# Optimization experiments

Hardware: AMD Instinct MI355X
Metric: run time of the kernel (lower is better)

The kernel has to match this reference:

```python
import jax, jax.numpy as jnp
import numpy as np

B, N, DS, DP, H, DH = 2, 512, 384, 128, 16, 64
MAX_SEQ = 2048
DI = H * DH  # inner attention dim = 1024
LN_EPS = 1e-5


def setup_inputs() -> dict:
    key = jax.random.key(0)
    ks = jax.random.split(key, 10)
    s = 0.02  # param init scale
    return {
        "single_repr": jax.random.normal(ks[0], (B, N, DS), jnp.float32),
        "pairwise_repr": jax.random.normal(ks[1], (B, N, N, DP), jnp.float32),
        "ln_gamma": jnp.ones((DP,), jnp.float32),
        "ln_beta": jnp.zeros((DP,), jnp.float32),
        "w_bias": jax.random.normal(ks[2], (DP, H), jnp.float32) * s,
        "attn_bias_bias": jax.random.normal(ks[3], (MAX_SEQ, MAX_SEQ), jnp.float32) * s,
        "w_q": jax.random.normal(ks[4], (DS, DI), jnp.float32) * s,
        "w_k": jax.random.normal(ks[5], (DS, DI), jnp.float32) * s,
        "w_v": jax.random.normal(ks[6], (DS, DI), jnp.float32) * s,
        "w_g": jax.random.normal(ks[7], (DS, DI), jnp.float32) * s,
        "w_o": jax.random.normal(ks[8], (DI, DS), jnp.float32) * s,
    }


def reference(single_repr, pairwise_repr, ln_gamma, ln_beta, w_bias,
              attn_bias_bias, w_q, w_k, w_v, w_g, w_o):
    b, n, _ = single_repr.shape
    # LayerNorm over pairwise feature dim, then project to per-head bias
    mu = pairwise_repr.mean(-1, keepdims=True)
    var = pairwise_repr.var(-1, keepdims=True)
    pr = (pairwise_repr - mu) * jax.lax.rsqrt(var + LN_EPS) * ln_gamma + ln_beta
    # ... i j h -> ... h i j, plus learned positional bias slice
    attn_bias = jnp.einsum('bijd,dh->bhij', pr, w_bias) + attn_bias_bias[:n, :n]

    # multi-head attention with additive per-head bias and sigmoid gating
    q = (single_repr @ w_q).reshape(b, n, H, DH).transpose(0, 2, 1, 3)  # bhnd
    k = (single_repr @ w_k).reshape(b, n, H, DH).transpose(0, 2, 1, 3)
    v = (single_repr @ w_v).reshape(b, n, H, DH).transpose(0, 2, 1, 3)
    scale = DH ** -0.5
    scores = jnp.einsum('bhid,bhjd->bhij', q, k) * scale + attn_bias
    attn = jax.nn.softmax(scores, axis=-1)
    o = jnp.einsum('bhij,bhjd->bhid', attn, v)
    o = o.transpose(0, 2, 1, 3).reshape(b, n, DI)
    gates = jax.nn.sigmoid(single_repr @ w_g)
    return (o * gates) @ w_o
```

## Files before the change

kernel.cpp:

```cpp
#include <hip/hip_runtime.h>
#include <hip/hip_bf16.h>

#define B_ 2
#define N_ 512
#define DS_ 384
#define DP_ 128
#define H_ 16
#define DH_ 64
#define DI_ 1024
#define MAXSEQ 2048
#define PAD 8

typedef float f32x4 __attribute__((ext_vector_type(4)));
typedef short bf16x8 __attribute__((ext_vector_type(8)));
typedef unsigned int u32x4 __attribute__((ext_vector_type(4)));

__device__ __forceinline__ unsigned short f2b(float f) {
    unsigned int u = __builtin_bit_cast(unsigned int, f);
    u += 0x7FFFu + ((u >> 16) & 1u);
    return (unsigned short)(u >> 16);
}
__device__ __forceinline__ float b2f(unsigned short s) {
    unsigned int u = ((unsigned int)s) << 16;
    return __builtin_bit_cast(float, u);
}

#define SW(row, bc) ((bc) ^ (((row) & 7) << 4))

__global__ __launch_bounds__(256) void k_pre(const float* __restrict__ pw,
                                             const float* __restrict__ abb,
                                             const float* __restrict__ gamma,
                                             const float* __restrict__ beta,
                                             const float* __restrict__ wb,
                                             const float* __restrict__ wq,
                                             const float* __restrict__ wk,
                                             const float* __restrict__ wv,
                                             const float* __restrict__ wg,
                                             const float* __restrict__ wo,
                                             unsigned short* __restrict__ Wt,
                                             unsigned short* __restrict__ Wot,
                                             unsigned short* __restrict__ biasP) {
    __shared__ float Xs[64 * 128];
    __shared__ float rsum[4][16] __attribute__((aligned(16)));
    __shared__ float rsq[4][16] __attribute__((aligned(16)));
    int bid = blockIdx.x;
    int t = threadIdx.x;

    if (bid >= 8192) {
        int tid = bid - 8192;
        int z = tid / 384, r = tid % 384;
        const float* in; unsigned short* out; int C, Rr, c0, r0;
        if (z < 4) {
            in = (z == 0) ? wq : (z == 1) ? wk : (z == 2) ? wv : wg;
            out = Wt + (long)z * 1024 * 384;
            C = 1024; Rr = 384;
            c0 = (r & 31) * 32; r0 = (r >> 5) * 32;
        } else {
            in = wo; out = Wot; C = 384; Rr = 1024;
            c0 = (r % 12) * 32; r0 = (r / 12) * 32;
        }
        float (*tile)[33] = (float(*)[33])Xs;
        int tx = t & 31, ty = t >> 5;
        #pragma unroll
        for (int i = ty; i < 32; i += 8)
            tile[i][tx] = in[(long)(r0 + i) * C + (c0 + tx)];
        __syncthreads();
        #pragma unroll
        for (int i = ty; i < 32; i += 8)
            out[(long)(c0 + i) * Rr + (r0 + tx)] = f2b(tile[tx][i]);
        return;
    }

    int w = t >> 6, lane = t & 63;
    int lane15 = lane & 15, kg = lane >> 4;
    long p0 = (long)bid * 64;
    int i_blk = (int)((p0 >> 9) & (N_ - 1));
    int j0 = (int)(p0 & (N_ - 1));
    long bb = p0 >> 18;

    const char* src = (const char*)(pw + (p0 << 7));
    char* lds = (char*)Xs;
    #pragma unroll
    for (int c = 0; c < 8; ++c) {
        int L = c * 4096 + t * 16;
        int row = L >> 9, b = L & 511;
        u32x4 v = __builtin_nontemporal_load((const u32x4*)(src + L));
        *(u32x4*)(lds + (row << 9) + (b ^ ((row & 7) << 4))) = v;
    }

    float shp = 0.f, thp = 0.f;
    bf16x8 gb[4];
    #pragma unroll
    for (int kk = 0; kk < 4; ++kk) {
        bf16x8 a;
        unsigned short* ap = (unsigned short*)&a;
        #pragma unroll
        for (int e = 0; e < 8; ++e) {
            int d = kk * 32 + kg * 8 + e;
            float wv_ = wb[d * 16 + lane15];
            float gv = gamma[d];
            ap[e] = f2b(gv * wv_);
            shp = fmaf(gv, wv_, shp);
            thp = fmaf(beta[d], wv_, thp);
        }
        gb[kk] = a;
    }
    shp += __shfl_xor(shp, 16); shp += __shfl_xor(shp, 32);
    thp += __shfl_xor(thp, 16); thp += __shfl_xor(thp, 32);
    float sh = shp, th = thp;
    __syncthreads();

    int row = w * 16 + lane15;
    const char* rbase = lds + (row << 9);
    int sw = (lane15 & 7) << 4;
    f32x4 xa[4], xb4[4];
    #pragma unroll
    for (int kk = 0; kk < 4; ++kk) {
        int b0 = kk * 128 + kg * 32;
        xa[kk]  = *(const f32x4*)(rbase + ((b0) ^ sw));
        xb4[kk] = *(const f32x4*)(rbase + ((b0 + 16) ^ sw));
    }
    float s = 0.f, q = 0.f;
    #pragma unroll
    for (int kk = 0; kk < 4; ++kk) {
        s += xa[kk][0] + xa[kk][1] + xa[kk][2] + xa[kk][3];
        s += xb4[kk][0] + xb4[kk][1] + xb4[kk][2] + xb4[kk][3];
        #pragma unroll
        for (int e = 0; e < 4; ++e) {
            q = fmaf(xa[kk][e], xa[kk][e], q);
            q = fmaf(xb4[kk][e], xb4[kk][e], q);
        }
    }
    s += __shfl_xor(s, 16); s += __shfl_xor(s, 32);
    q += __shfl_xor(q, 16); q += __shfl_xor(q, 32);
    if (lane < 16) { rsum[w][lane15] = s; rsq[w][lane15] = q; }

    f32x4 acc = {};
    #pragma unroll
    for (int kk = 0; kk < 4; ++kk) {
        bf16x8 a;
        unsigned short* ap = (unsigned short*)&a;
        ap[0] = f2b(xa[kk][0]);  ap[1] = f2b(xa[kk][1]);
        ap[2] = f2b(xa[kk][2]);  ap[3] = f2b(xa[kk][3]);
        ap[4] = f2b(xb4[kk][0]); ap[5] = f2b(xb4[kk][1]);
        ap[6] = f2b(xb4[kk][2]); ap[7] = f2b(xb4[kk][3]);
        acc = __builtin_amdgcn_mfma_f32_16x16x32_bf16(a, gb[kk], acc, 0, 0, 0);
    }
    int jr = w * 16 + kg * 4;
    float4 rs = *(const float4*)&rsum[w][kg * 4];
    float4 rq = *(const float4*)&rsq[w][kg * 4];
    float4 av = *(const float4*)(abb + (long)i_blk * MAXSEQ + j0 + jr);
    unsigned short* planeBase = biasP + ((bb * H_ + lane15) * N_ + i_blk) * N_ + j0;
    ushort4 res;
    float mu, var;
    mu = rs.x * (1.f / DP_); var = fmaf(rq.x, 1.f / DP_, -mu * mu);
    res.x = f2b(fmaf(rsqrtf(var + 1e-5f), acc[0] - mu * sh, th + av.x));
    mu = rs.y * (1.f / DP_); var = fmaf(rq.y, 1.f / DP_, -mu * mu);
    res.y = f2b(fmaf(rsqrtf(var + 1e-5f), acc[1] - mu * sh, th + av.y));
    mu = rs.z * (1.f / DP_); var = fmaf(rq.z, 1.f / DP_, -mu * mu);
    res.z = f2b(fmaf(rsqrtf(var + 1e-5f), acc[2] - mu * sh, th + av.z));
    mu = rs.w * (1.f / DP_); var = fmaf(rq.w, 1.f / DP_, -mu * mu);
    res.w = f2b(fmaf(rsqrtf(var + 1e-5f), acc[3] - mu * sh, th + av.w));
    *(ushort4*)(planeBase + jr) = res;
}

__global__ __launch_bounds__(256) void k_proj(const float* __restrict__ X,
                                              const unsigned short* __restrict__ Wt,
                                              unsigned short* __restrict__ Qb,
                                              unsigned short* __restrict__ Kb,
                                              unsigned short* __restrict__ Vt,
                                              unsigned short* __restrict__ Xg) {
    __shared__ unsigned short As[64][64 + PAD];
    __shared__ unsigned short Bs[128][64 + PAD];
    int m0 = blockIdx.x * 64;
    int n0 = blockIdx.y * 128;
    int t = threadIdx.x;
    int wave = t >> 6, lane = t & 63;
    int wr = wave >> 1, wc = wave & 1;
    int lane15 = lane & 15, kg = lane >> 4;
    int rA = t >> 2, qA = t & 3;
    int rB = t >> 1, hB = t & 1;
    f32x4 acc[2][4] = {};
    for (int k0 = 0; k0 < DS_; k0 += 64) {
        __syncthreads();
        {
            const float4* srcA = (const float4*)(X + (long)(m0 + rA) * DS_ + k0 + qA * 16);
            unsigned short* dstA = &As[rA][qA * 16];
            #pragma unroll
            for (int ii = 0; ii < 4; ++ii) {
                float4 v = srcA[ii];
                dstA[ii * 4 + 0] = f2b(v.x); dstA[ii * 4 + 1] = f2b(v.y);
                dstA[ii * 4 + 2] = f2b(v.z); dstA[ii * 4 + 3] = f2b(v.w);
            }
            const uint4* srcB = (const uint4*)(Wt + (long)(n0 + rB) * DS_ + k0 + hB * 32);
            uint4* dstB = (uint4*)&Bs[rB][hB * 32];
            dstB[0] = srcB[0]; dstB[1] = srcB[1]; dstB[2] = srcB[2]; dstB[3] = srcB[3];
        }
        __syncthreads();
        #pragma unroll
        for (int ks = 0; ks < 2; ++ks) {
            bf16x8 a[2], bbv[4];
            #pragma unroll
            for (int mf = 0; mf < 2; ++mf)
                a[mf] = *(const bf16x8*)&As[wr * 32 + mf * 16 + lane15][ks * 32 + kg * 8];
            #pragma unroll
            for (int nf = 0; nf < 4; ++nf)
                bbv[nf] = *(const bf16x8*)&Bs[wc * 64 + nf * 16 + lane15][ks * 32 + kg * 8];
            #pragma unroll
            for (int mf = 0; mf < 2; ++mf)
                #pragma unroll
                for (int nf = 0; nf < 4; ++nf)
                    acc[mf][nf] = __builtin_amdgcn_mfma_f32_16x16x32_bf16(a[mf], bbv[nf], acc[mf][nf], 0, 0, 0);
        }
    }
    int p = n0 >> 10;
    int lgrp = lane >> 4;
    #pragma unroll
    for (int mf = 0; mf < 2; ++mf) {
        #pragma unroll
        for (int nf = 0; nf < 4; ++nf) {
            int col = n0 + wc * 64 + nf * 16 + lane15;
            int ch = col & 1023;
            int h = ch >> 6, dh = ch & 63;
            int row0 = m0 + wr * 32 + mf * 16 + lgrp * 4;
            if (p == 0 || p == 1) {
                unsigned short* base = (p == 0) ? Qb : Kb;
                float scl = (p == 0) ? 0.125f : 1.0f;
                #pragma unroll
                for (int rr = 0; rr < 4; ++rr) {
                    int rowx = row0 + rr;
                    int b = rowx >> 9, n = rowx & 511;
                    base[(((long)(b * 16 + h)) * 512 + n) * 64 + dh] = f2b(acc[mf][nf][rr] * scl);
                }
            } else if (p == 2) {
                int b = row0 >> 9, n = row0 & 511;
                ushort4 v;
                v.x = f2b(acc[mf][nf][0]); v.y = f2b(acc[mf][nf][1]);
                v.z = f2b(acc[mf][nf][2]); v.w = f2b(acc[mf][nf][3]);
                *(ushort4*)&Vt[(((long)(b * 16 + h)) * 64 + dh) * 512 + n] = v;
            } else {
                #pragma unroll
                for (int rr = 0; rr < 4; ++rr) {
                    int rowx = row0 + rr;
                    Xg[(long)rowx * 1024 + ch] = f2b(acc[mf][nf][rr]);
                }
            }
        }
    }
}

__global__ __launch_bounds__(512) void k_flash(const unsigned short* __restrict__ Qb,
                                               const unsigned short* __restrict__ Kb,
                                               const unsigned short* __restrict__ Vt,
                                               const unsigned short* __restrict__ biasP,
                                               const unsigned short* __restrict__ Xg,
                                               unsigned short* __restrict__ Og) {
    __shared__ unsigned short Kt[2][64][64];
    __shared__ unsigned short Vs[2][64][64];
    __shared__ unsigned short Bt[2][64][64];
    __shared__ char PsOscr[16384];
    __shared__ float Mscr[4][16], Lscr[4][16];
    unsigned short (*Ps)[16][64] = (unsigned short(*)[16][64])PsOscr;
    float (*Oscr)[16][64] = (float(*)[16][64])PsOscr;
    int bh = blockIdx.y;
    int b = bh >> 4, h = bh & 15;
    int i0 = blockIdx.x * 64;
    int t = threadIdx.x, w = t >> 6, lane = t & 63;
    int g = w & 3, jg = w >> 2;
    int lane15 = lane & 15, lgrp = lane >> 4;
    int tl = t & 255;
    int rs_ = tl >> 3, cs_ = tl & 7;

    bf16x8 qf[2];
    #pragma unroll
    for (int kk = 0; kk < 2; ++kk)
        qf[kk] = *(const bf16x8*)&Qb[((long)bh * 512 + i0 + g * 16 + lane15) * 64 + kk * 32 + lgrp * 8];

    float m_run = -1e30f, l_run = 0.f;
    f32x4 o[4] = {};

    for (int jtl = 0; jtl < 4; ++jtl) {
        int j0 = (jg * 4 + jtl) * 64;
        __syncthreads();
        {
            int r2 = rs_ + 32;
            *(uint4*)((char*)&Kt[jg][rs_][0] + SW(rs_, cs_ * 16)) =
                *(const uint4*)&Kb[((long)bh * 512 + j0 + rs_) * 64 + cs_ * 8];
            *(uint4*)((char*)&Vs[jg][rs_][0] + SW(rs_, cs_ * 16)) =
                *(const uint4*)&Vt[((long)bh * 64 + rs_) * 512 + j0 + cs_ * 8];
            *(uint4*)((char*)&Bt[jg][rs_][0] + SW(rs_, cs_ * 16)) =
                *(const uint4*)&biasP[((long)bh * 512 + i0 + rs_) * 512 + j0 + cs_ * 8];
            *(uint4*)((char*)&Kt[jg][r2][0] + SW(r2, cs_ * 16)) =
                *(const uint4*)&Kb[((long)bh * 512 + j0 + r2) * 64 + cs_ * 8];
            *(uint4*)((char*)&Vs[jg][r2][0] + SW(r2, cs_ * 16)) =
                *(const uint4*)&Vt[((long)bh * 64 + r2) * 512 + j0 + cs_ * 8];
            *(uint4*)((char*)&Bt[jg][r2][0] + SW(r2, cs_ * 16)) =
                *(const uint4*)&biasP[((long)bh * 512 + i0 + r2) * 512 + j0 + cs_ * 8];
        }
        __syncthreads();

        f32x4 s[4];
        #pragma unroll
        for (int nf = 0; nf < 4; ++nf) {
            f32x4 z = {};
            #pragma unroll
            for (int kk = 0; kk < 2; ++kk) {
                bf16x8 af = *(const bf16x8*)((const char*)&Kt[jg][nf * 16 + lane15][0] +
                                             SW(lane15, kk * 64 + lgrp * 16));
                z = __builtin_amdgcn_mfma_f32_16x16x32_bf16(af, qf[kk], z, 0, 0, 0);
            }
            s[nf] = z;
        }
        #pragma unroll
        for (int nf = 0; nf < 4; ++nf) {
            ushort4 bv = *(const ushort4*)((const char*)&Bt[jg][g * 16 + lane15][0] +
                                           SW(lane15, nf * 32 + lgrp * 8));
            s[nf][0] += b2f(bv.x); s[nf][1] += b2f(bv.y);
            s[nf][2] += b2f(bv.z); s[nf][3] += b2f(bv.w);
        }

        float pmax = s[0][0];
        #pragma unroll
        for (int nf = 0; nf < 4; ++nf)
            #pragma unroll
            for (int rr = 0; rr < 4; ++rr) pmax = fmaxf(pmax, s[nf][rr]);
        pmax = fmaxf(pmax, __shfl_xor(pmax, 16));
        pmax = fmaxf(pmax, __shfl_xor(pmax, 32));
        float m_new = fmaxf(m_run, pmax);
        float scale = __expf(m_run - m_new);
        float psum = 0.f;
        #pragma unroll
        for (int nf = 0; nf < 4; ++nf)
            #pragma unroll
            for (int rr = 0; rr < 4; ++rr) {
                s[nf][rr] = __expf(s[nf][rr] - m_new);
                psum += s[nf][rr];
            }
        psum += __shfl_xor(psum, 16);
        psum += __shfl_xor(psum, 32);
        l_run = l_run * scale + psum;
        m_run = m_new;
        #pragma unroll
        for (int rr = 0; rr < 4; ++rr) {
            float sc = __shfl(scale, lgrp * 4 + rr);
            #pragma unroll
            for (int nf = 0; nf < 4; ++nf) o[nf][rr] *= sc;
        }
        #pragma unroll
        for (int nf = 0; nf < 4; ++nf) {
            ushort4 pv_;
            pv_.x = f2b(s[nf][0]); pv_.y = f2b(s[nf][1]);
            pv_.z = f2b(s[nf][2]); pv_.w = f2b(s[nf][3]);
            *(ushort4*)((char*)&Ps[w][lane15][0] + SW(lane15, nf * 32 + lgrp * 8)) = pv_;
        }
        #pragma unroll
        for (int kk = 0; kk < 2; ++kk) {
            bf16x8 pa = *(const bf16x8*)((const char*)&Ps[w][lane15][0] +
                                         SW(lane15, kk * 64 + lgrp * 16));
            #pragma unroll
            for (int nf = 0; nf < 4; ++nf) {
                bf16x8 vb = *(const bf16x8*)((const char*)&Vs[jg][nf * 16 + lane15][0] +
                                             SW(lane15, kk * 64 + lgrp * 16));
                o[nf] = __builtin_amdgcn_mfma_f32_16x16x32_bf16(pa, vb, o[nf], 0, 0, 0);
            }
        }
    }

    __syncthreads();
    if (jg == 1) {
        if (lane < 16) { Mscr[g][lane] = m_run; Lscr[g][lane] = l_run; }
        #pragma unroll
        for (int nf = 0; nf < 4; ++nf)
            #pragma unroll
            for (int rr = 0; rr < 4; ++rr)
                Oscr[g][lgrp * 4 + rr][nf * 16 + lane15] = o[nf][rr];
    }
    __syncthreads();
    if (jg == 0) {
        #pragma unroll
        for (int rr = 0; rr < 4; ++rr) {
            int row = lgrp * 4 + rr;
            float m1 = __shfl(m_run, row);
            float l1 = __shfl(l_run, row);
            float m2 = Mscr[g][row];
            float l2 = Lscr[g][row];
            float mm = fmaxf(m1, m2);
            float e1 = __expf(m1 - mm), e2 = __expf(m2 - mm);
            float inv = 1.f / (l1 * e1 + l2 * e2);
            long grow = (long)b * 512 + i0 + g * 16 + row;
            #pragma unroll
            for (int nf = 0; nf < 4; ++nf) {
                int dh = nf * 16 + lane15;
                float o2 = Oscr[g][row][dh];
                float val = (o[nf][rr] * e1 + o2 * e2) * inv;
                float xgv = b2f(Xg[grow * 1024 + h * 64 + dh]);
                float gate = 1.f / (1.f + __expf(-xgv));
                Og[grow * 1024 + h * 64 + dh] = f2b(val * gate);
            }
        }
    }
}

__global__ __launch_bounds__(256) void k_out(const unsigned short* __restrict__ Og,
                                             const unsigned short* __restrict__ Wot,
                                             float* __restrict__ out) {
    __shared__ unsigned short As[64][64 + PAD];
    __shared__ unsigned short Bs[64][64 + PAD];
    int m0 = blockIdx.x * 64, n0 = blockIdx.y * 64;
    int t = threadIdx.x, wave = t >> 6, lane = t & 63;
    int wr = wave >> 1, wc = wave & 1;
    int lane15 = lane & 15, kg = lane >> 4;
    f32x4 acc[2][2] = {};
    for (int k0 = 0; k0 < 1024; k0 += 64) {
        __syncthreads();
        {
            int r = t >> 2, qd = t & 3;
            const uint4* s1 = (const uint4*)(Og + (long)(m0 + r) * 1024 + k0 + qd * 16);
            uint4* d1 = (uint4*)&As[r][qd * 16];
            d1[0] = s1[0]; d1[1] = s1[1];
            const uint4* s2 = (const uint4*)(Wot + (long)(n0 + r) * 1024 + k0 + qd * 16);
            uint4* d2 = (uint4*)&Bs[r][qd * 16];
            d2[0] = s2[0]; d2[1] = s2[1];
        }
        __syncthreads();
        #pragma unroll
        for (int ks = 0; ks < 2; ++ks) {
            bf16x8 a[2], bbv[2];
            #pragma unroll
            for (int mf = 0; mf < 2; ++mf)
                a[mf] = *(const bf16x8*)&As[wr * 32 + mf * 16 + lane15][ks * 32 + kg * 8];
            #pragma unroll
            for (int nf = 0; nf < 2; ++nf)
                bbv[nf] = *(const bf16x8*)&Bs[wc * 32 + nf * 16 + lane15][ks * 32 + kg * 8];
            #pragma unroll
            for (int mf = 0; mf < 2; ++mf)
                #pragma unroll
                for (int nf = 0; nf < 2; ++nf)
                    acc[mf][nf] = __builtin_amdgcn_mfma_f32_16x16x32_bf16(a[mf], bbv[nf], acc[mf][nf], 0, 0, 0);
        }
    }
    int lgrp = lane >> 4;
    #pragma unroll
    for (int mf = 0; mf < 2; ++mf) {
        #pragma unroll
        for (int nf = 0; nf < 2; ++nf) {
            int col = n0 + wc * 32 + nf * 16 + lane15;
            int row0 = m0 + wr * 32 + mf * 16 + lgrp * 4;
            #pragma unroll
            for (int rr = 0; rr < 4; ++rr)
                out[(long)(row0 + rr) * DS_ + col] = acc[mf][nf][rr];
        }
    }
}

extern "C" void kernel_launch(void* const* d_in, const int* in_sizes, int n_in,
                              void* d_out, int out_size, void* d_ws, size_t ws_size,
                              hipStream_t stream) {
    const float* single = (const float*)d_in[0];
    const float* pw     = (const float*)d_in[1];
    const float* gamma  = (const float*)d_in[2];
    const float* beta   = (const float*)d_in[3];
    const float* wb     = (const float*)d_in[4];
    const float* abb    = (const float*)d_in[5];
    const float* wq     = (const float*)d_in[6];
    const float* wk     = (const float*)d_in[7];
    const float* wv     = (const float*)d_in[8];
    const float* wg     = (const float*)d_in[9];
    const float* wo     = (const float*)d_in[10];
    float* out = (float*)d_out;
    char* ws = (char*)d_ws;

    unsigned short* SP  = (unsigned short*)(ws);
    unsigned short* Qb  = (unsigned short*)(ws + 16777216);
    unsigned short* Kb  = (unsigned short*)(ws + 18874368);
    unsigned short* Vt  = (unsigned short*)(ws + 20971520);
    unsigned short* Xg  = (unsigned short*)(ws + 23068672);
    unsigned short* Og  = (unsigned short*)(ws + 25165824);
    unsigned short* Wt  = (unsigned short*)(ws + 27262976);
    unsigned short* Wot = (unsigned short*)(ws + 30408704);

    k_pre<<<10112, 256, 0, stream>>>(pw, abb, gamma, beta, wb,
                                     wq, wk, wv, wg, wo, Wt, Wot, SP);
    k_proj<<<dim3(16, 32), 256, 0, stream>>>(single, Wt, Qb, Kb, Vt, Xg);
    k_flash<<<dim3(8, 32), 512, 0, stream>>>(Qb, Kb, Vt, SP, Xg, Og);
    k_out<<<dim3(16, 6), 256, 0, stream>>>(Og, Wot, out);
}
```

Baseline: 114.2 us.

## Make k_pre LayerNorm-bias waves persistent with register double-buffered pairwise loads

The pairwise LayerNorm+bias-projection part of k_pre now launches 1024 blocks instead of 8192. Each wave independently processes eight 16-row tiles, strided by 4096 tiles, using its own LDS slice. While computing the current tile it prefetches the next tile into registers, overlapping HBM loads with compute. It also drops the block-wide __syncthreads and amortizes the gamma/w_bias setup across tiles, at the cost of extra registers and fewer in-flight blocks.

Measured after the change: 112.8 us. About the same (-1.2%).

```diff
diff --git a/kernel.cpp b/kernel.cpp
--- a/kernel.cpp
+++ b/kernel.cpp
@@ -40,14 +40,14 @@
                                              unsigned short* __restrict__ Wt,
                                              unsigned short* __restrict__ Wot,
                                              unsigned short* __restrict__ biasP) {
-    __shared__ float Xs[64 * 128];
-    __shared__ float rsum[4][16] __attribute__((aligned(16)));
-    __shared__ float rsq[4][16] __attribute__((aligned(16)));
+    __shared__ float Xs4[4][16 * 128];
+    __shared__ float rsum4[4][16] __attribute__((aligned(16)));
+    __shared__ float rsq4[4][16] __attribute__((aligned(16)));
     int bid = blockIdx.x;
     int t = threadIdx.x;
 
-    if (bid >= 8192) {
-        int tid = bid - 8192;
+    if (bid >= 1024) {
+        int tid = bid - 1024;
         int z = tid / 384, r = tid % 384;
         const float* in; unsigned short* out; int C, Rr, c0, r0;
         if (z < 4) {
@@ -59,7 +59,7 @@
             in = wo; out = Wot; C = 384; Rr = 1024;
             c0 = (r % 12) * 32; r0 = (r / 12) * 32;
         }
-        float (*tile)[33] = (float(*)[33])Xs;
+        float (*tile)[33] = (float(*)[33])&Xs4[0][0];
         int tx = t & 31, ty = t >> 5;
         #pragma unroll
         for (int i = ty; i < 32; i += 8)
@@ -73,20 +73,6 @@
 
     int w = t >> 6, lane = t & 63;
     int lane15 = lane & 15, kg = lane >> 4;
-    long p0 = (long)bid * 64;
-    int i_blk = (int)((p0 >> 9) & (N_ - 1));
-    int j0 = (int)(p0 & (N_ - 1));
-    long bb = p0 >> 18;
-
-    const char* src = (const char*)(pw + (p0 << 7));
-    char* lds = (char*)Xs;
-    #pragma unroll
-    for (int c = 0; c < 8; ++c) {
-        int L = c * 4096 + t * 16;
-        int row = L >> 9, b = L & 511;
-        u32x4 v = __builtin_nontemporal_load((const u32x4*)(src + L));
-        *(u32x4*)(lds + (row << 9) + (b ^ ((row & 7) << 4))) = v;
-    }
 
     float shp = 0.f, thp = 0.f;
     bf16x8 gb[4];
@@ -108,60 +94,92 @@
     shp += __shfl_xor(shp, 16); shp += __shfl_xor(shp, 32);
     thp += __shfl_xor(thp, 16); thp += __shfl_xor(thp, 32);
     float sh = shp, th = thp;
-    __syncthreads();
-
-    int row = w * 16 + lane15;
-    const char* rbase = lds + (row << 9);
-    int sw = (lane15 & 7) << 4;
-    f32x4 xa[4], xb4[4];
-    #pragma unroll
-    for (int kk = 0; kk < 4; ++kk) {
-        int b0 = kk * 128 + kg * 32;
-        xa[kk]  = *(const f32x4*)(rbase + ((b0) ^ sw));
-        xb4[kk] = *(const f32x4*)(rbase + ((b0 + 16) ^ sw));
-    }
-    float s = 0.f, q = 0.f;
-    #pragma unroll
-    for (int kk = 0; kk < 4; ++kk) {
-        s += xa[kk][0] + xa[kk][1] + xa[kk][2] + xa[kk][3];
-        s += xb4[kk][0] + xb4[kk][1] + xb4[kk][2] + xb4[kk][3];
-        #pragma unroll
-        for (int e = 0; e < 4; ++e) {
-            q = fmaf(xa[kk][e], xa[kk][e], q);
-            q = fmaf(xb4[kk][e], xb4[kk][e], q);
-        }
-    }
-    s += __shfl_xor(s, 16); s += __shfl_xor(s, 32);
-    q += __shfl_xor(q, 16); q += __shfl_xor(q, 32);
-    if (lane < 16) { rsum[w][lane15] = s; rsq[w][lane15] = q; }
-
-    f32x4 acc = {};
-    #pragma unroll
-    for (int kk = 0; kk < 4; ++kk) {
-        bf16x8 a;
-        unsigned short* ap = (unsigned short*)&a;
-        ap[0] = f2b(xa[kk][0]);  ap[1] = f2b(xa[kk][1]);
-        ap[2] = f2b(xa[kk][2]);  ap[3] = f2b(xa[kk][3]);
-        ap[4] = f2b(xb4[kk][0]); ap[5] = f2b(xb4[kk][1]);
-        ap[6] = f2b(xb4[kk][2]); ap[7] = f2b(xb4[kk][3]);
-        acc = __builtin_amdgcn_mfma_f32_16x16x32_bf16(a, gb[kk], acc, 0, 0, 0);
-    }
-    int jr = w * 16 + kg * 4;
-    float4 rs = *(const float4*)&rsum[w][kg * 4];
-    float4 rq = *(const float4*)&rsq[w][kg * 4];
-    float4 av = *(const float4*)(abb + (long)i_blk * MAXSEQ + j0 + jr);
-    unsigned short* planeBase = biasP + ((bb * H_ + lane15) * N_ + i_blk) * N_ + j0;
-    ushort4 res;
-    float mu, var;
-    mu = rs.x * (1.f / DP_); var = fmaf(rq.x, 1.f / DP_, -mu * mu);
-    res.x = f2b(fmaf(rsqrtf(var + 1e-5f), acc[0] - mu * sh, th + av.x));
-    mu = rs.y * (1.f / DP_); var = fmaf(rq.y, 1.f / DP_, -mu * mu);
-    res.y = f2b(fmaf(rsqrtf(var + 1e-5f), acc[1] - mu * sh, th + av.y));
-    mu = rs.z * (1.f / DP_); var = fmaf(rq.z, 1.f / DP_, -mu * mu);
-    res.z = f2b(fmaf(rsqrtf(var + 1e-5f), acc[2] - mu * sh, th + av.z));
-    mu = rs.w * (1.f / DP_); var = fmaf(rq.w, 1.f / DP_, -mu * mu);
-    res.w = f2b(fmaf(rsqrtf(var + 1e-5f), acc[3] - mu * sh, th + av.w));
-    *(ushort4*)(planeBase + jr) = res;
+
+    char* lds = (char*)&Xs4[w][0];
+    float* rsum = rsum4[w];
+    float* rsq  = rsq4[w];
+    long wstream = (long)bid * 4 + w;
+
+    u32x4 rg[8];
+    {
+        const char* src0 = (const char*)pw + (wstream << 13);
+        #pragma unroll
+        for (int c = 0; c < 8; ++c)
+            rg[c] = __builtin_nontemporal_load((const u32x4*)(src0 + c * 1024 + lane * 16));
+    }
+
+    for (int s = 0; s < 8; ++s) {
+        long tile = wstream + (long)s * 4096;
+        long p0 = tile * 16;
+        int i_blk = (int)((p0 >> 9) & (N_ - 1));
+        int j0 = (int)(p0 & (N_ - 1));
+        long bb = p0 >> 18;
+
+        #pragma unroll
+        for (int c = 0; c < 8; ++c) {
+            int L = c * 1024 + lane * 16;
+            int row = L >> 9, b = L & 511;
+            *(u32x4*)(lds + (row << 9) + (b ^ ((row & 7) << 4))) = rg[c];
+        }
+        if (s < 7) {
+            const char* srcn = (const char*)pw + ((tile + 4096) << 13);
+            #pragma unroll
+            for (int c = 0; c < 8; ++c)
+                rg[c] = __builtin_nontemporal_load((const u32x4*)(srcn + c * 1024 + lane * 16));
+        }
+
+        const char* rbase = lds + (lane15 << 9);
+        int sw = (lane15 & 7) << 4;
+        f32x4 xa[4], xb4[4];
+        #pragma unroll
+        for (int kk = 0; kk < 4; ++kk) {
+            int b0 = kk * 128 + kg * 32;
+            xa[kk]  = *(const f32x4*)(rbase + ((b0) ^ sw));
+            xb4[kk] = *(const f32x4*)(rbase + ((b0 + 16) ^ sw));
+        }
+        float s_ = 0.f, q = 0.f;
+        #pragma unroll
+        for (int kk = 0; kk < 4; ++kk) {
+            s_ += xa[kk][0] + xa[kk][1] + xa[kk][2] + xa[kk][3];
+            s_ += xb4[kk][0] + xb4[kk][1] + xb4[kk][2] + xb4[kk][3];
+            #pragma unroll
+            for (int e = 0; e < 4; ++e) {
+                q = fmaf(xa[kk][e], xa[kk][e], q);
+                q = fmaf(xb4[kk][e], xb4[kk][e], q);
+            }
+        }
+        s_ += __shfl_xor(s_, 16); s_ += __shfl_xor(s_, 32);
+        q  += __shfl_xor(q, 16);  q  += __shfl_xor(q, 32);
+        if (lane < 16) { rsum[lane15] = s_; rsq[lane15] = q; }
+
+        f32x4 acc = {};
+        #pragma unroll
+        for (int kk = 0; kk < 4; ++kk) {
+            bf16x8 a;
+            unsigned short* ap = (unsigned short*)&a;
+            ap[0] = f2b(xa[kk][0]);  ap[1] = f2b(xa[kk][1]);
+            ap[2] = f2b(xa[kk][2]);  ap[3] = f2b(xa[kk][3]);
+            ap[4] = f2b(xb4[kk][0]); ap[5] = f2b(xb4[kk][1]);
+            ap[6] = f2b(xb4[kk][2]); ap[7] = f2b(xb4[kk][3]);
+            acc = __builtin_amdgcn_mfma_f32_16x16x32_bf16(a, gb[kk], acc, 0, 0, 0);
+        }
+        int jr = kg * 4;
+        float4 rs = *(const float4*)&rsum[jr];
+        float4 rq = *(const float4*)&rsq[jr];
+        float4 av = *(const float4*)(abb + (long)i_blk * MAXSEQ + j0 + jr);
+        unsigned short* planeBase = biasP + ((bb * H_ + lane15) * N_ + i_blk) * N_ + j0;
+        ushort4 res;
+        float mu, var;
+        mu = rs.x * (1.f / DP_); var = fmaf(rq.x, 1.f / DP_, -mu * mu);
+        res.x = f2b(fmaf(rsqrtf(var + 1e-5f), acc[0] - mu * sh, th + av.x));
+        mu = rs.y * (1.f / DP_); var = fmaf(rq.y, 1.f / DP_, -mu * mu);
+        res.y = f2b(fmaf(rsqrtf(var + 1e-5f), acc[1] - mu * sh, th + av.y));
+        mu = rs.z * (1.f / DP_); var = fmaf(rq.z, 1.f / DP_, -mu * mu);
+        res.z = f2b(fmaf(rsqrtf(var + 1e-5f), acc[2] - mu * sh, th + av.z));
+        mu = rs.w * (1.f / DP_); var = fmaf(rq.w, 1.f / DP_, -mu * mu);
+        res.w = f2b(fmaf(rsqrtf(var + 1e-5f), acc[3] - mu * sh, th + av.w));
+        *(ushort4*)(planeBase + jr) = res;
+    }
 }
 
 __global__ __launch_bounds__(256) void k_proj(const float* __restrict__ X,
@@ -479,8 +497,8 @@
     unsigned short* Wt  = (unsigned short*)(ws + 27262976);
     unsigned short* Wot = (unsigned short*)(ws + 30408704);
 
-    k_pre<<<10112, 256, 0, stream>>>(pw, abb, gamma, beta, wb,
-                                     wq, wk, wv, wg, wo, Wt, Wot, SP);
+    k_pre<<<2944, 256, 0, stream>>>(pw, abb, gamma, beta, wb,
+                                    wq, wk, wv, wg, wo, Wt, Wot, SP);
     k_proj<<<dim3(16, 32), 256, 0, stream>>>(single, Wt, Qb, Kb, Vt, Xg);
     k_flash<<<dim3(8, 32), 512, 0, stream>>>(Qb, Kb, Vt, SP, Xg, Og);
     k_out<<<dim3(16, 6), 256, 0, stream>>>(Og, Wot, out);
```
